# Kernel tuning notes

Measured on AMD Instinct MI355X. Metric: run time of the kernel, lower is better.

Reference implementation:

```python
import jax, jax.numpy as jnp
import numpy as np

MIN_DELAY = 60
MAX_DELAY = 420
TAU = 0.0          # module's self.tau (min magnitude for resonant_activation)
TEMPERATURE = 1.0  # forward() default gumbel-softmax temperature


def setup_inputs() -> dict:
    key = jax.random.key(0)
    k1, k2, k3, k4 = jax.random.split(key, 4)
    B, T = 128, 8192
    excitation = jax.random.normal(k1, (B, 1, T), dtype=jnp.float32)
    u = jax.random.uniform(k2, (MAX_DELAY - MIN_DELAY,), dtype=jnp.float32,
                           minval=1e-6, maxval=1.0 - 1e-6)
    gumbel_noise = -jnp.log(-jnp.log(u))  # standard Gumbel samples
    delay_param = jax.random.normal(k3, (MAX_DELAY - MIN_DELAY,), dtype=jnp.float32)
    feedback_gain = jnp.ones((1,), dtype=jnp.float32)
    reflection_coeffs = jax.random.normal(k4, (2,), dtype=jnp.float32)
    return {"excitation": excitation, "gumbel_noise": gumbel_noise,
            "delay_param": delay_param, "feedback_gain": feedback_gain,
            "reflection_coeffs": reflection_coeffs}


def _resonant_activation(x, min_magnitude):
    sign = jnp.sign(x)
    magnitude = jnp.abs(jnp.tanh(x))
    return sign * (min_magnitude + (1.0 - min_magnitude) * magnitude)


def _build_coeffs(gumbel_noise, delay_param, feedback_gain, reflection_coeffs):
    # gumbel_softmax(tau=TEMPERATURE, hard=True) with straight-through estimator
    logits = (delay_param + gumbel_noise) / TEMPERATURE
    soft = jax.nn.softmax(logits)
    hard = jax.nn.one_hot(jnp.argmax(soft), soft.shape[0], dtype=soft.dtype)
    one_hot = jax.lax.stop_gradient(hard - soft) + soft
    shifted = jnp.roll(one_hot, 1)
    # low_pass_bias=False -> tanh, then resonant_activation (applies tanh again, as in source)
    rc = jnp.tanh(reflection_coeffs)
    k1 = _resonant_activation(rc[0], TAU)
    k2 = _resonant_activation(rc[1], TAU)
    a1 = k1 * (1.0 - k2)
    a2 = jnp.clip(k2, -0.999, 0.999)
    a1_bound = 0.999 - jnp.abs(a2)
    a1 = jnp.clip(a1, -a1_bound, a1_bound)
    g = jax.nn.sigmoid(feedback_gain[0]) ** 0.45
    a1 = a1 * g
    a2 = a2 * g
    tail = one_hot * a1 + shifted * a2               # [max_delay - min_delay]
    coeffs = jnp.concatenate([jnp.zeros((MIN_DELAY,), tail.dtype), tail])  # [max_delay]
    return coeffs


def _sample_wise_lpc(x, coeffs):
    # All-pole IIR: y[t] = x[t] - sum_{i=0}^{D-1} coeffs[i] * y[t-1-i]
    B, T = x.shape
    D = coeffs.shape[0]
    buf0 = jnp.zeros((B, D), x.dtype)  # buf[:, i] = y[t-1-i]

    def step(buf, x_t):
        y_t = x_t - buf @ coeffs                              # [B]
        buf = jnp.concatenate([y_t[:, None], buf[:, :-1]], 1)  # shift delay line
        return buf, y_t

    _, ys = jax.lax.scan(step, buf0, x.T)  # ys: [T, B]
    return ys.T


def reference(excitation, gumbel_noise, delay_param, feedback_gain, reflection_coeffs):
    coeffs = _build_coeffs(gumbel_noise, delay_param, feedback_gain, reflection_coeffs)
    x = excitation[:, 0, :]                 # [B, T]
    y = _sample_wise_lpc(x, coeffs)         # [B, T]
    return y[:, None, :]                    # [B, 1, T]
```

## Files before the change

kernel.cpp:

```cpp
#include <hip/hip_runtime.h>
#include <cmath>

#define T_LEN 8192
#define B_ROWS 128
#define ND 360
#define MIN_DELAY_C 60

__global__ __launch_bounds__(64) void ks_resonator_kernel(
    const float* __restrict__ excitation,
    const float* __restrict__ gumbel,
    const float* __restrict__ delay_param,
    const float* __restrict__ feedback_gain,
    const float* __restrict__ refl,
    float* __restrict__ out)
{
    __shared__ float y[T_LEN];

    const int lane = threadIdx.x;
    const int row  = blockIdx.x;

    float best = -INFINITY;
    int   bi   = 0;
    for (int i = lane; i < ND; i += 64) {
        float v = delay_param[i] + gumbel[i];
        if (v > best) { best = v; bi = i; }
    }
    #pragma unroll
    for (int off = 32; off > 0; off >>= 1) {
        float v2 = __shfl_xor(best, off);
        int   i2 = __shfl_xor(bi, off);
        if (v2 > best || (v2 == best && i2 < bi)) { best = v2; bi = i2; }
    }
    const int p = bi;

    float k1 = tanhf(tanhf(refl[0]));
    float k2 = tanhf(tanhf(refl[1]));
    float a1 = k1 * (1.0f - k2);
    float a2 = fminf(fmaxf(k2, -0.999f), 0.999f);
    float bound = 0.999f - fabsf(a2);
    a1 = fminf(fmaxf(a1, -bound), bound);
    float g = powf(1.0f / (1.0f + expf(-feedback_gain[0])), 0.45f);
    a1 *= g; a2 *= g;

    const int lagA = MIN_DELAY_C + p + 1;
    const int lagB = MIN_DELAY_C + ((p + 1) % ND) + 1;
    const int C    = (lagA < lagB) ? lagA : lagB;

    const float4* xv = (const float4*)(excitation + (size_t)row * T_LEN);
    float4*       yv = (float4*)y;
    #pragma unroll 8
    for (int i = 0; i < T_LEN / 4 / 64; i++)
        yv[i * 64 + lane] = xv[i * 64 + lane];

    for (int pos = 0; pos < T_LEN; pos += C) {
        int end = pos + C; if (end > T_LEN) end = T_LEN;
        for (int j = pos + lane; j < end; j += 64) {
            float ya = (j >= lagA) ? y[j - lagA] : 0.0f;
            float yb = (j >= lagB) ? y[j - lagB] : 0.0f;
            y[j] = y[j] - a1 * ya - a2 * yb;
        }
    }

    float4* ov = (float4*)(out + (size_t)row * T_LEN);
    #pragma unroll 8
    for (int i = 0; i < T_LEN / 4 / 64; i++)
        ov[i * 64 + lane] = yv[i * 64 + lane];
}

extern "C" void kernel_launch(void* const* d_in, const int* in_sizes, int n_in,
                              void* d_out, int out_size, void* d_ws, size_t ws_size,
                              hipStream_t stream) {
    const float* excitation    = (const float*)d_in[0];
    const float* gumbel        = (const float*)d_in[1];
    const float* delay_param   = (const float*)d_in[2];
    const float* feedback_gain = (const float*)d_in[3];
    const float* refl          = (const float*)d_in[4];
    float* out = (float*)d_out;

    ks_resonator_kernel<<<B_ROWS, 64, 0, stream>>>(
        excitation, gumbel, delay_param, feedback_gain, refl, out);
}
```

Measured before the change: 82.96 us.

## Recast two-tap IIR as FIR pre-filters plus 8x-lag recursion with 512 threads

```diff
diff --git a/kernel.cpp b/kernel.cpp
--- a/kernel.cpp
+++ b/kernel.cpp
@@ -5,8 +5,9 @@
 #define B_ROWS 128
 #define ND 360
 #define MIN_DELAY_C 60
+#define BLOCK 512
 
-__global__ __launch_bounds__(64) void ks_resonator_kernel(
+__global__ __launch_bounds__(BLOCK) void ks_resonator_kernel(
     const float* __restrict__ excitation,
     const float* __restrict__ gumbel,
     const float* __restrict__ delay_param,
@@ -14,13 +15,14 @@
     const float* __restrict__ refl,
     float* __restrict__ out)
 {
-    __shared__ float y[T_LEN];
+    __shared__ float A[T_LEN];
+    __shared__ float Bv[T_LEN];
 
-    const int lane = threadIdx.x;
+    const int tid  = threadIdx.x;
+    const int lane = tid & 63;
     const int row  = blockIdx.x;
 
-    float best = -INFINITY;
-    int   bi   = 0;
+    float best = -INFINITY; int bi = 0;
     for (int i = lane; i < ND; i += 64) {
         float v = delay_param[i] + gumbel[i];
         if (v > best) { best = v; bi = i; }
@@ -28,7 +30,7 @@
     #pragma unroll
     for (int off = 32; off > 0; off >>= 1) {
         float v2 = __shfl_xor(best, off);
-        int   i2 = __shfl_xor(bi, off);
+        int   i2 = __shfl_xor(bi,   off);
         if (v2 > best || (v2 == best && i2 < bi)) { best = v2; bi = i2; }
     }
     const int p = bi;
@@ -37,34 +39,94 @@
     float k2 = tanhf(tanhf(refl[1]));
     float a1 = k1 * (1.0f - k2);
     float a2 = fminf(fmaxf(k2, -0.999f), 0.999f);
-    float bound = 0.999f - fabsf(a2);
-    a1 = fminf(fmaxf(a1, -bound), bound);
+    float bnd = 0.999f - fabsf(a2);
+    a1 = fminf(fmaxf(a1, -bnd), bnd);
     float g = powf(1.0f / (1.0f + expf(-feedback_gain[0])), 0.45f);
     a1 *= g; a2 *= g;
 
-    const int lagA = MIN_DELAY_C + p + 1;
-    const int lagB = MIN_DELAY_C + ((p + 1) % ND) + 1;
-    const int C    = (lagA < lagB) ? lagA : lagB;
+    const int dA = MIN_DELAY_C + p + 1;
+    const int dB = MIN_DELAY_C + ((p + 1) % ND) + 1;
 
     const float4* xv = (const float4*)(excitation + (size_t)row * T_LEN);
-    float4*       yv = (float4*)y;
-    #pragma unroll 8
-    for (int i = 0; i < T_LEN / 4 / 64; i++)
-        yv[i * 64 + lane] = xv[i * 64 + lane];
+    float4* Av4 = (float4*)A;
+    #pragma unroll
+    for (int i = 0; i < T_LEN / 4 / BLOCK; i++)
+        Av4[i * BLOCK + tid] = xv[i * BLOCK + tid];
+    __syncthreads();
 
-    for (int pos = 0; pos < T_LEN; pos += C) {
-        int end = pos + C; if (end > T_LEN) end = T_LEN;
-        for (int j = pos + lane; j < end; j += 64) {
-            float ya = (j >= lagA) ? y[j - lagA] : 0.0f;
-            float yb = (j >= lagB) ? y[j - lagB] : 0.0f;
-            y[j] = y[j] - a1 * ya - a2 * yb;
+    {
+        const float c0 = -a1, c1 = -a2;
+        for (int t = tid; t < T_LEN; t += BLOCK) {
+            float s = A[t];
+            if (t >= dA) s += c0 * A[t - dA];
+            if (t >= dB) s += c1 * A[t - dB];
+            Bv[t] = s;
+        }
+    }
+    __syncthreads();
+
+    {
+        const float c0 = a1 * a1, c1 = 2.f * a1 * a2, c2 = a2 * a2;
+        const int  d0 = 2 * dA,  d1 = dA + dB,       d2 = 2 * dB;
+        for (int t = tid; t < T_LEN; t += BLOCK) {
+            float s = Bv[t];
+            if (t >= d0) s += c0 * Bv[t - d0];
+            if (t >= d1) s += c1 * Bv[t - d1];
+            if (t >= d2) s += c2 * Bv[t - d2];
+            A[t] = s;
+        }
+    }
+    __syncthreads();
+
+    {
+        const float a1_2 = a1 * a1, a2_2 = a2 * a2;
+        const float c0 = a1_2 * a1_2, c1 = 4.f * a1_2 * a1 * a2,
+                    c2 = 6.f * a1_2 * a2_2, c3 = 4.f * a1 * a2 * a2_2,
+                    c4 = a2_2 * a2_2;
+        const int d0 = 4 * dA, d1 = 3 * dA + dB, d2 = 2 * (dA + dB),
+                  d3 = dA + 3 * dB, d4 = 4 * dB;
+        for (int t = tid; t < T_LEN; t += BLOCK) {
+            float s = A[t];
+            if (t >= d0) s += c0 * A[t - d0];
+            if (t >= d1) s += c1 * A[t - d1];
+            if (t >= d2) s += c2 * A[t - d2];
+            if (t >= d3) s += c3 * A[t - d3];
+            if (t >= d4) s += c4 * A[t - d4];
+            Bv[t] = s;
+        }
+    }
+    __syncthreads();
+
+    {
+        float c[9]; int d[9];
+        const float binom[9] = {1.f, 8.f, 28.f, 56.f, 70.f, 56.f, 28.f, 8.f, 1.f};
+        #pragma unroll
+        for (int i = 0; i <= 8; i++) {
+            float pa = 1.f, pb = 1.f;
+            for (int j = 0; j < 8 - i; j++) pa *= a1;
+            for (int j = 0; j < i; j++)     pb *= a2;
+            c[i] = binom[i] * pa * pb;
+            d[i] = (8 - i) * dA + i * dB;
+        }
+        const int chunk = 8 * (dA < dB ? dA : dB);
+        for (int pos = 0; pos < T_LEN; pos += chunk) {
+            int end = pos + chunk; if (end > T_LEN) end = T_LEN;
+            for (int t = pos + tid; t < end; t += BLOCK) {
+                float s = Bv[t];
+                #pragma unroll
+                for (int i = 0; i <= 8; i++)
+                    if (t >= d[i]) s += c[i] * Bv[t - d[i]];
+                Bv[t] = s;
+            }
+            __syncthreads();
         }
     }
 
     float4* ov = (float4*)(out + (size_t)row * T_LEN);
-    #pragma unroll 8
-    for (int i = 0; i < T_LEN / 4 / 64; i++)
-        ov[i * 64 + lane] = yv[i * 64 + lane];
+    const float4* Bv4 = (const float4*)Bv;
+    #pragma unroll
+    for (int i = 0; i < T_LEN / 4 / BLOCK; i++)
+        ov[i * BLOCK + tid] = Bv4[i * BLOCK + tid];
 }
 
 extern "C" void kernel_launch(void* const* d_in, const int* in_sizes, int n_in,
@@ -77,6 +139,6 @@
     const float* refl          = (const float*)d_in[4];
     float* out = (float*)d_out;
 
-    ks_resonator_kernel<<<B_ROWS, 64, 0, stream>>>(
+    ks_resonator_kernel<<<B_ROWS, BLOCK, 0, stream>>>(
         excitation, gumbel, delay_param, feedback_gain, refl, out);
 }
```

Measured after the change: 83.19 us. Within noise of the previous version (+0.3%).
